# Kernel tuning notes

Measured on AMD Instinct MI355X. Metric: run time of the kernel, lower is better.

## Reference

```python
import jax, jax.numpy as jnp
import numpy as np
from jax import lax

B, T, K = 4096, 512, 2048  # students, timesteps, skills


def setup_inputs() -> dict:
    key = jax.random.key(0)
    k1, k2, k3 = jax.random.split(key, 3)
    skills = jax.random.randint(k1, (B, T), 0, K, dtype=jnp.int32)
    responses = (jax.random.uniform(k2, (B, T)) < 0.7).astype(jnp.float32)
    kp = jax.random.split(k3, 4)
    k0 = jax.random.uniform(kp[0], (K,), minval=0.05, maxval=0.85)  # initial mastery per skill
    t = jax.random.uniform(kp[1], (K,), minval=0.01, maxval=0.30)   # transit
    g = jax.random.uniform(kp[2], (K,), minval=0.05, maxval=0.30)   # guess
    s = jax.random.uniform(kp[3], (K,), minval=0.01, maxval=0.10)   # slip
    return {"skills": skills, "responses": responses, "k0": k0, "t": t, "g": g, "s": s, "num_skills": K}


def _bkt_forward(skills, responses, k0, t, g, s, num_skills):
    # Batched BKT inter_predict: per-student per-skill mastery recurrence.
    Bb, Tt = skills.shape
    rows = jnp.arange(Bb)

    def step(carry, xs):
        last, seen = carry              # [B, K] mastery state, [B, K] seen mask
        sk, res = xs                    # [B] skill ids, [B] responses at this timestep
        lm = last[rows, sk]             # gather current per-skill mastery
        sn = seen[rows, sk]
        kk = k0[sk]; tt = t[sk]; gg = g[sk]; ss = s[sk]
        # first time a skill is seen -> prior k0, else last posterior
        pL = jnp.where(sn, lm, kk)
        # Bayesian posterior given observed response
        p_corr = pL * (1.0 - ss) / (pL * (1.0 - ss) + (1.0 - pL) * gg)
        p_inc = pL * ss / (pL * ss + (1.0 - pL) * (1.0 - gg))
        p = jnp.where(res == 1.0, p_corr, p_inc)
        nxt = p + (1.0 - p) * tt        # learning transition
        last = last.at[rows, sk].set(nxt)
        seen = seen.at[rows, sk].set(True)
        return (last, seen), pL          # emitted mastery BEFORE update (as in original)

    init = (jnp.zeros((Bb, num_skills), responses.dtype),
            jnp.zeros((Bb, num_skills), dtype=bool))
    _, mastery = lax.scan(step, init, (skills.T, responses.T))  # [T, B]
    return mastery.T  # [B, T]


def reference(skills, responses, k0, t, g, s, num_skills):
    return _bkt_forward(skills, responses, k0, t, g, s, num_skills)
```

## Files before the change

kernel.cpp:

```cpp
#include <hip/hip_runtime.h>
#include <limits.h>


#define BKT_B 4096
#define BKT_T 512
#define BKT_K 2048
#define BLK   256
#define TPT   (BKT_T / BLK)
#define HASH  1024
#define PTR_END 0x3FF

__device__ __forceinline__ float bkt_update(float p, int rbit, float ss,
                                            float gg, float tt) {
  float num, den;
  if (rbit) {
    num = p * (1.0f - ss);
    den = num + (1.0f - p) * gg;
  } else {
    num = p * ss;
    den = num + (1.0f - p) * (1.0f - gg);
  }
  const float q = num / den;
  return q + (1.0f - q) * tt;
}

__global__ __launch_bounds__(BLK) void bkt_kernel(
    const int* __restrict__ skills,
    const float* __restrict__ resp,
    const float* __restrict__ k0,
    const float* __restrict__ tp,
    const float* __restrict__ gp,
    const float* __restrict__ sp,
    float* __restrict__ out) {
  __shared__ int head_s[HASH];
  __shared__ int node_s[BKT_T];

  const int b = blockIdx.x;
  const int base = b * BKT_T;
  const int tid = threadIdx.x;

  int   sk[TPT];
  float rr[TPT];
  float k0v[TPT];
#pragma unroll
  for (int u = 0; u < TPT; ++u) {
    const int t = tid + u * BLK;
    sk[u] = skills[base + t];
    rr[u] = resp[base + t];
  }
#pragma unroll
  for (int u = 0; u < TPT; ++u)
    k0v[u] = k0[sk[u]];

  ((int4*)head_s)[tid] = make_int4(-1, -1, -1, -1);
  __syncthreads();

#pragma unroll
  for (int u = 0; u < TPT; ++u) {
    const int t = tid + u * BLK;
    const int s_ = sk[u];
    const int old = atomicExch(&head_s[s_ & (HASH - 1)], t);
    const int ptr = (old < 0) ? PTR_END : old;
    const int rbit = rr[u] > 0.5f ? 1 : 0;
    node_s[t] = ptr | (rbit << 10) | (s_ << 11);
  }
  __syncthreads();

#pragma unroll
  for (int u = 0; u < TPT; ++u) {
    const int t = tid + u * BLK;
    const int s_ = sk[u];
    const int head = head_s[s_ & (HASH - 1)];

    int rank = 0, minj = INT_MAX, minnode = 0;
    for (int j = head; j >= 0; ) {
      const int node = node_s[j];
      if (j < t && (node >> 11) == s_) {
        ++rank;
        if (j < minj) { minj = j; minnode = node; }
      }
      const int nx = node & PTR_END;
      j = (nx == PTR_END) ? -1 : nx;
    }

    float p = k0v[u];

    if (rank > 0) {
      const float ss = sp[s_];
      const float gg = gp[s_];
      const float tt = tp[s_];
      p = bkt_update(p, (minnode >> 10) & 1, ss, gg, tt);
      int cur = minj;
      for (int rd = 1; rd < rank; ++rd) {
        int best = INT_MAX, bestnode = 0;
        for (int j = head; j >= 0; ) {
          const int node = node_s[j];
          if (j < t && j > cur && (node >> 11) == s_ && j < best) {
            best = j; bestnode = node;
          }
          const int nx = node & PTR_END;
          j = (nx == PTR_END) ? -1 : nx;
        }
        p = bkt_update(p, (bestnode >> 10) & 1, ss, gg, tt);
        cur = best;
      }
    }

    out[base + t] = p;
  }
}

extern "C" void kernel_launch(void* const* d_in, const int* in_sizes, int n_in,
                              void* d_out, int out_size, void* d_ws, size_t ws_size,
                              hipStream_t stream) {
  const int*   skills = (const int*)d_in[0];
  const float* resp   = (const float*)d_in[1];
  const float* k0     = (const float*)d_in[2];
  const float* tp     = (const float*)d_in[3];
  const float* gp     = (const float*)d_in[4];
  const float* sp     = (const float*)d_in[5];
  float* out = (float*)d_out;

  bkt_kernel<<<BKT_B, BLK, 0, stream>>>(skills, resp, k0, tp, gp, sp, out);
}
```

Measured before the change: 15.19 us.

## Replace hash-chained linked lists with per-bucket time bitmaps for BKT replay

Swaps the shared-memory hash table of linked lists for a 16x256 bitmap indexed by 32-step time word and skill bucket, plus packed response bits gathered with wave ballots. Each timestep now walks set bits in earlier time words in order, so prior occurrences arrive already sorted and the repeated min-search passes over the chain go away. The cost is a fixed scan of up to 16 bitmap words per thread and more shared memory (16KB+), which may lower occupancy.

```diff
diff --git a/kernel.cpp b/kernel.cpp
--- a/kernel.cpp
+++ b/kernel.cpp
@@ -1,5 +1,4 @@
 #include <hip/hip_runtime.h>
-#include <limits.h>
 
 
 #define BKT_B 4096
@@ -7,8 +6,8 @@
 #define BKT_K 2048
 #define BLK   256
 #define TPT   (BKT_T / BLK)
-#define HASH  1024
-#define PTR_END 0x3FF
+#define NB    256
+#define NW    (BKT_T / 32)
 
 __device__ __forceinline__ float bkt_update(float p, int rbit, float ss,
                                             float gg, float tt) {
@@ -32,8 +31,9 @@
     const float* __restrict__ gp,
     const float* __restrict__ sp,
     float* __restrict__ out) {
-  __shared__ int head_s[HASH];
-  __shared__ int node_s[BKT_T];
+  __shared__ unsigned int   bmap_s[NW][NB];
+  __shared__ unsigned short sk_s[BKT_T];
+  __shared__ unsigned int   resp_s[NW];
 
   const int b = blockIdx.x;
   const int base = b * BKT_T;
@@ -52,17 +52,30 @@
   for (int u = 0; u < TPT; ++u)
     k0v[u] = k0[sk[u]];
 
-  ((int4*)head_s)[tid] = make_int4(-1, -1, -1, -1);
+  {
+    int4* z = (int4*)&bmap_s[0][0];
+#pragma unroll
+    for (int i = 0; i < 4; ++i)
+      z[tid + i * BLK] = make_int4(0, 0, 0, 0);
+  }
+
+#pragma unroll
+  for (int u = 0; u < TPT; ++u) {
+    const int t = tid + u * BLK;
+    sk_s[t] = (unsigned short)sk[u];
+    const unsigned long long m = __ballot(rr[u] > 0.5f);
+    if ((tid & 63) == 0) {
+      const int w0 = t >> 5;
+      resp_s[w0]     = (unsigned int)(m & 0xffffffffu);
+      resp_s[w0 + 1] = (unsigned int)(m >> 32);
+    }
+  }
   __syncthreads();
 
 #pragma unroll
   for (int u = 0; u < TPT; ++u) {
     const int t = tid + u * BLK;
-    const int s_ = sk[u];
-    const int old = atomicExch(&head_s[s_ & (HASH - 1)], t);
-    const int ptr = (old < 0) ? PTR_END : old;
-    const int rbit = rr[u] > 0.5f ? 1 : 0;
-    node_s[t] = ptr | (rbit << 10) | (s_ << 11);
+    atomicOr(&bmap_s[t >> 5][sk[u] & (NB - 1)], 1u << (t & 31));
   }
   __syncthreads();
 
@@ -70,39 +83,27 @@
   for (int u = 0; u < TPT; ++u) {
     const int t = tid + u * BLK;
     const int s_ = sk[u];
-    const int head = head_s[s_ & (HASH - 1)];
-
-    int rank = 0, minj = INT_MAX, minnode = 0;
-    for (int j = head; j >= 0; ) {
-      const int node = node_s[j];
-      if (j < t && (node >> 11) == s_) {
-        ++rank;
-        if (j < minj) { minj = j; minnode = node; }
-      }
-      const int nx = node & PTR_END;
-      j = (nx == PTR_END) ? -1 : nx;
-    }
+    const int bucket = s_ & (NB - 1);
+    const int wt = t >> 5;
 
     float p = k0v[u];
+    float ss = 0.f, gg = 0.f, tt = 0.f;
+    bool have = false;
 
-    if (rank > 0) {
-      const float ss = sp[s_];
-      const float gg = gp[s_];
-      const float tt = tp[s_];
-      p = bkt_update(p, (minnode >> 10) & 1, ss, gg, tt);
-      int cur = minj;
-      for (int rd = 1; rd < rank; ++rd) {
-        int best = INT_MAX, bestnode = 0;
-        for (int j = head; j >= 0; ) {
-          const int node = node_s[j];
-          if (j < t && j > cur && (node >> 11) == s_ && j < best) {
-            best = j; bestnode = node;
+    for (int w = 0; w <= wt; ++w) {
+      unsigned int bits = bmap_s[w][bucket];
+      if (w == wt) bits &= (1u << (t & 31)) - 1u;
+      while (bits) {
+        const int j = (w << 5) + __builtin_ctz(bits);
+        bits &= bits - 1;
+        if (sk_s[j] == (unsigned short)s_) {
+          if (!have) {
+            ss = sp[s_]; gg = gp[s_]; tt = tp[s_];
+            have = true;
           }
-          const int nx = node & PTR_END;
-          j = (nx == PTR_END) ? -1 : nx;
+          const unsigned int rw = resp_s[j >> 5];
+          p = bkt_update(p, (int)((rw >> (j & 31)) & 1u), ss, gg, tt);
         }
-        p = bkt_update(p, (bestnode >> 10) & 1, ss, gg, tt);
-        cur = best;
       }
     }
 
```

New measurement: 32.88 us. 2.16x slower.

## Map one student per wavefront and interleave two chain walks per lane

Applied to the files above, without the earlier changes.

Each 64-lane wavefront now processes a whole student, with per-wave hash tables of 256 buckets, so the block-level __syncthreads barriers go away and the launch uses a quarter as many blocks. Each lane handles eight timesteps and walks two hash chains at once to overlap LDS latency. The first walk also records the two smallest earlier indices, which saves a rescan for rank two. Risks are longer chains from the smaller hash, more register pressure, and relying on wave-synchronous LDS visibility without an explicit barrier.

```diff
diff --git a/kernel.cpp b/kernel.cpp
--- a/kernel.cpp
+++ b/kernel.cpp
@@ -6,8 +6,9 @@
 #define BKT_T 512
 #define BKT_K 2048
 #define BLK   256
-#define TPT   (BKT_T / BLK)
-#define HASH  1024
+#define WPB   4
+#define TPL   8
+#define HASH  256
 #define PTR_END 0x3FF
 
 __device__ __forceinline__ float bkt_update(float p, int rbit, float ss,
@@ -24,7 +25,7 @@
   return q + (1.0f - q) * tt;
 }
 
-__global__ __launch_bounds__(BLK) void bkt_kernel(
+__global__ void bkt_kernel(
     const int* __restrict__ skills,
     const float* __restrict__ resp,
     const float* __restrict__ k0,
@@ -32,81 +33,125 @@
     const float* __restrict__ gp,
     const float* __restrict__ sp,
     float* __restrict__ out) {
-  __shared__ int head_s[HASH];
-  __shared__ int node_s[BKT_T];
+  __shared__ int head_s[WPB][HASH];
+  __shared__ int node_s[WPB][BKT_T];
 
-  const int b = blockIdx.x;
-  const int base = b * BKT_T;
-  const int tid = threadIdx.x;
+  const int wid  = threadIdx.x >> 6;
+  const int lane = threadIdx.x & 63;
+  const int stu  = blockIdx.x * WPB + wid;
+  const int base = stu * BKT_T;
 
-  int   sk[TPT];
-  float rr[TPT];
-  float k0v[TPT];
+  int sk[TPL], rb[TPL];
 #pragma unroll
-  for (int u = 0; u < TPT; ++u) {
-    const int t = tid + u * BLK;
+  for (int u = 0; u < TPL; ++u) {
+    const int t = lane + 64 * u;
     sk[u] = skills[base + t];
-    rr[u] = resp[base + t];
+    rb[u] = resp[base + t] > 0.5f ? 1 : 0;
   }
+
+  ((int4*)&head_s[wid][0])[lane] = make_int4(-1, -1, -1, -1);
+  __builtin_amdgcn_sched_barrier(0);
+
 #pragma unroll
-  for (int u = 0; u < TPT; ++u)
+  for (int u = 0; u < TPL; ++u) {
+    const int t = lane + 64 * u;
+    const int s_ = sk[u];
+    const int old = atomicExch(&head_s[wid][s_ & (HASH - 1)], t);
+    node_s[wid][t] = ((old < 0) ? PTR_END : old) | (rb[u] << 10) | (s_ << 11);
+  }
+  __builtin_amdgcn_sched_barrier(0);
+
+  float k0v[TPL];
+#pragma unroll
+  for (int u = 0; u < TPL; ++u)
     k0v[u] = k0[sk[u]];
 
-  ((int4*)head_s)[tid] = make_int4(-1, -1, -1, -1);
-  __syncthreads();
+#pragma unroll
+  for (int c = 0; c < TPL / 2; ++c) {
+    const int ua = 2 * c, ub = 2 * c + 1;
+    const int ta = lane + 64 * ua, tb = lane + 64 * ub;
+    const int sa = sk[ua], sb = sk[ub];
+    const int heada = head_s[wid][sa & (HASH - 1)];
+    const int headb = head_s[wid][sb & (HASH - 1)];
 
-#pragma unroll
-  for (int u = 0; u < TPT; ++u) {
-    const int t = tid + u * BLK;
-    const int s_ = sk[u];
-    const int old = atomicExch(&head_s[s_ & (HASH - 1)], t);
-    const int ptr = (old < 0) ? PTR_END : old;
-    const int rbit = rr[u] > 0.5f ? 1 : 0;
-    node_s[t] = ptr | (rbit << 10) | (s_ << 11);
-  }
-  __syncthreads();
-
-#pragma unroll
-  for (int u = 0; u < TPT; ++u) {
-    const int t = tid + u * BLK;
-    const int s_ = sk[u];
-    const int head = head_s[s_ & (HASH - 1)];
-
-    int rank = 0, minj = INT_MAX, minnode = 0;
-    for (int j = head; j >= 0; ) {
-      const int node = node_s[j];
-      if (j < t && (node >> 11) == s_) {
-        ++rank;
-        if (j < minj) { minj = j; minnode = node; }
+    int ja = heada, jb = headb;
+    int ranka = 0, rankb = 0;
+    int a1 = INT_MAX, a2 = INT_MAX, an1 = 0, an2 = 0;
+    int b1 = INT_MAX, b2 = INT_MAX, bn1 = 0, bn2 = 0;
+    while ((ja >= 0) || (jb >= 0)) {
+      if (ja >= 0) {
+        const int nd = node_s[wid][ja];
+        if (ja < ta && (nd >> 11) == sa) {
+          ++ranka;
+          if (ja < a1)      { a2 = a1; an2 = an1; a1 = ja; an1 = nd; }
+          else if (ja < a2) { a2 = ja; an2 = nd; }
+        }
+        const int nx = nd & PTR_END;
+        ja = (nx == PTR_END) ? -1 : nx;
       }
-      const int nx = node & PTR_END;
-      j = (nx == PTR_END) ? -1 : nx;
-    }
-
-    float p = k0v[u];
-
-    if (rank > 0) {
-      const float ss = sp[s_];
-      const float gg = gp[s_];
-      const float tt = tp[s_];
-      p = bkt_update(p, (minnode >> 10) & 1, ss, gg, tt);
-      int cur = minj;
-      for (int rd = 1; rd < rank; ++rd) {
-        int best = INT_MAX, bestnode = 0;
-        for (int j = head; j >= 0; ) {
-          const int node = node_s[j];
-          if (j < t && j > cur && (node >> 11) == s_ && j < best) {
-            best = j; bestnode = node;
-          }
-          const int nx = node & PTR_END;
-          j = (nx == PTR_END) ? -1 : nx;
+      if (jb >= 0) {
+        const int nd = node_s[wid][jb];
+        if (jb < tb && (nd >> 11) == sb) {
+          ++rankb;
+          if (jb < b1)      { b2 = b1; bn2 = bn1; b1 = jb; bn1 = nd; }
+          else if (jb < b2) { b2 = jb; bn2 = nd; }
         }
-        p = bkt_update(p, (bestnode >> 10) & 1, ss, gg, tt);
-        cur = best;
+        const int nx = nd & PTR_END;
+        jb = (nx == PTR_END) ? -1 : nx;
       }
     }
 
-    out[base + t] = p;
+    float pa = k0v[ua];
+    if (ranka > 0) {
+      const float ss = sp[sa];
+      const float gg = gp[sa];
+      const float tt = tp[sa];
+      pa = bkt_update(pa, (an1 >> 10) & 1, ss, gg, tt);
+      if (ranka > 1) {
+        pa = bkt_update(pa, (an2 >> 10) & 1, ss, gg, tt);
+        int cur = a2;
+        for (int rd = 2; rd < ranka; ++rd) {
+          int best = INT_MAX, bestnode = 0;
+          for (int j = heada; j >= 0; ) {
+            const int nd = node_s[wid][j];
+            if (j < ta && j > cur && j < best && (nd >> 11) == sa) {
+              best = j; bestnode = nd;
+            }
+            const int nx = nd & PTR_END;
+            j = (nx == PTR_END) ? -1 : nx;
+          }
+          pa = bkt_update(pa, (bestnode >> 10) & 1, ss, gg, tt);
+          cur = best;
+        }
+      }
+    }
+    out[base + ta] = pa;
+
+    float pb = k0v[ub];
+    if (rankb > 0) {
+      const float ss = sp[sb];
+      const float gg = gp[sb];
+      const float tt = tp[sb];
+      pb = bkt_update(pb, (bn1 >> 10) & 1, ss, gg, tt);
+      if (rankb > 1) {
+        pb = bkt_update(pb, (bn2 >> 10) & 1, ss, gg, tt);
+        int cur = b2;
+        for (int rd = 2; rd < rankb; ++rd) {
+          int best = INT_MAX, bestnode = 0;
+          for (int j = headb; j >= 0; ) {
+            const int nd = node_s[wid][j];
+            if (j < tb && j > cur && j < best && (nd >> 11) == sb) {
+              best = j; bestnode = nd;
+            }
+            const int nx = nd & PTR_END;
+            j = (nx == PTR_END) ? -1 : nx;
+          }
+          pb = bkt_update(pb, (bestnode >> 10) & 1, ss, gg, tt);
+          cur = best;
+        }
+      }
+    }
+    out[base + tb] = pb;
   }
 }
 
@@ -121,5 +166,5 @@
   const float* sp     = (const float*)d_in[5];
   float* out = (float*)d_out;
 
-  bkt_kernel<<<BKT_B, BLK, 0, stream>>>(skills, resp, k0, tp, gp, sp, out);
+  bkt_kernel<<<BKT_B / WPB, BLK, 0, stream>>>(skills, resp, k0, tp, gp, sp, out);
 }
```

Measured after the change: 23.75 us. +56.3%, slower.
